# Performance work log

Hardware: AMD Instinct MI355X
Metric: run time of the kernel (lower is better)

## Reference

```python
import jax, jax.numpy as jnp
import numpy as np

N = 4096      # n_nodes
F = 512       # input_dim
R = 64        # repr_dim
H = 8         # n_heads
EPS_BIAS = 0.01
ALPHA = 0.2   # LeakyReLU negative slope
NEG_BIG = 1e16


def setup_inputs() -> dict:
    key = jax.random.key(0)
    k1, k2, k3, k4, k5 = jax.random.split(key, 5)
    node_matrix = jax.random.normal(k1, (N, F), dtype=jnp.float32)
    adjacency_matrix = (jax.random.uniform(k2, (N, N)) < 0.01).astype(jnp.float32)
    adjacency_matrix = jnp.maximum(adjacency_matrix, jnp.eye(N, dtype=jnp.float32))
    # learned parameters (xavier-ish scale)
    W = jax.random.normal(k3, (H, F, R), dtype=jnp.float32) * 0.06
    shared_attention = jax.random.normal(k4, (H, 2 * R), dtype=jnp.float32) * 0.1
    attention_biases = jax.random.normal(k5, (N, N), dtype=jnp.float32) * 0.02
    return {
        "node_matrix": node_matrix,
        "adjacency_matrix": adjacency_matrix,
        "W": W,
        "shared_attention": shared_attention,
        "attention_biases": attention_biases,
    }


def reference(node_matrix, adjacency_matrix, W, shared_attention, attention_biases):
    # hidden_repr: [H, N, R]
    hidden = jnp.einsum('nf,hfr->hnr', node_matrix, W)
    # per-head source/destination scores: [H, N]
    a_src = jnp.einsum('hnr,hr->hn', hidden, shared_attention[:, :R])
    a_dst = jnp.einsum('hnr,hr->hn', hidden, shared_attention[:, R:])
    # broadcast-sum + trainable pair bias: [H, N, N]
    pre = a_src[:, :, None] + a_dst[:, None, :] + EPS_BIAS * attention_biases[None]
    full = jnp.where(pre >= 0, pre, ALPHA * pre)  # LeakyReLU
    # adjacency masking then row softmax
    scores = full + (-NEG_BIG * (1.0 - adjacency_matrix))[None]
    att = jax.nn.softmax(scores, axis=-1)  # [H, N, N]
    # weighted aggregation: [H, N, R]
    out = jnp.einsum('hnm,hmr->hnr', att, hidden)
    # 'concat' aggregation: [N, H*R], head h occupies columns h*R:(h+1)*R
    return jnp.transpose(out, (1, 0, 2)).reshape(N, H * R)
```

## Files before the change

### kernel.cpp

```cpp
#include <hip/hip_runtime.h>
#include <hip/hip_bf16.h>

#define NN 4096
#define FF 512
#define RR 64
#define HH 8
#define HR (HH * RR)
#define CAP 128
#define ATT_STRIDE 144

typedef short bf16x8 __attribute__((ext_vector_type(8)));
typedef float f32x4 __attribute__((ext_vector_type(4)));

__device__ __forceinline__ unsigned short f2bf(float f) {
  __hip_bfloat16 h = __float2bfloat16(f);
  return *reinterpret_cast<unsigned short*>(&h);
}
__device__ __forceinline__ float bf2f(unsigned short u) {
  union { unsigned u32; float f; } cv;
  cv.u32 = ((unsigned)u) << 16;
  return cv.f;
}

__global__ __launch_bounds__(256) void k_convert(
    const float* __restrict__ X, const float* __restrict__ W,
    unsigned short* __restrict__ Xb, unsigned short* __restrict__ BbT)
{
  const int t = blockIdx.x * 256 + threadIdx.x;
  if (t < 524288) {
    const float4 v = reinterpret_cast<const float4*>(X)[t];
    ushort4 u;
    u.x = f2bf(v.x); u.y = f2bf(v.y); u.z = f2bf(v.z); u.w = f2bf(v.w);
    reinterpret_cast<ushort4*>(Xb)[t] = u;
  } else {
    const int o = t - 524288;
    const int n = o >> 9;
    const int f = o & 511;
    const int h = n >> 6, r = n & 63;
    BbT[(size_t)n * FF + f] = f2bf(W[(size_t)h * FF * RR + (size_t)f * RR + r]);
  }
}

__global__ __launch_bounds__(256) void k_gemm_hidden(
    const unsigned short* __restrict__ Xb,
    const unsigned short* __restrict__ BbT,
    unsigned short* __restrict__ hiddenT)
{
  const int row0 = blockIdx.x * 64;
  const int n0 = blockIdx.y * 64;
  __shared__ unsigned short Als[64 * 32];
  __shared__ unsigned short Bls[64 * 32];
  const int tid = threadIdx.x;
  const int l = tid & 63;
  const int wid = tid >> 6;
  const int wr = wid >> 1, wc = wid & 1;

  f32x4 acc[2][2];
#pragma unroll
  for (int a = 0; a < 2; ++a)
#pragma unroll
    for (int b = 0; b < 2; ++b) acc[a][b] = (f32x4){0.f, 0.f, 0.f, 0.f};

  const int srow = tid >> 2;
  const int skel = (tid & 3) * 8;

  for (int k0 = 0; k0 < FF; k0 += 32) {
    const int4 av = *reinterpret_cast<const int4*>(
        &Xb[(size_t)(row0 + srow) * FF + k0 + skel]);
    const int4 bv = *reinterpret_cast<const int4*>(
        &BbT[(size_t)(n0 + srow) * FF + k0 + skel]);
    __syncthreads();
    *reinterpret_cast<int4*>(&Als[tid * 8]) = av;
    *reinterpret_cast<int4*>(&Bls[tid * 8]) = bv;
    __syncthreads();

    const int ka = (l >> 4) * 8;
    const bf16x8 a0 = *reinterpret_cast<const bf16x8*>(&Als[(32 * wr + 0  + (l & 15)) * 32 + ka]);
    const bf16x8 a1 = *reinterpret_cast<const bf16x8*>(&Als[(32 * wr + 16 + (l & 15)) * 32 + ka]);
    const bf16x8 b0 = *reinterpret_cast<const bf16x8*>(&Bls[(32 * wc + 0  + (l & 15)) * 32 + ka]);
    const bf16x8 b1 = *reinterpret_cast<const bf16x8*>(&Bls[(32 * wc + 16 + (l & 15)) * 32 + ka]);
    acc[0][0] = __builtin_amdgcn_mfma_f32_16x16x32_bf16(a0, b0, acc[0][0], 0, 0, 0);
    acc[0][1] = __builtin_amdgcn_mfma_f32_16x16x32_bf16(a0, b1, acc[0][1], 0, 0, 0);
    acc[1][0] = __builtin_amdgcn_mfma_f32_16x16x32_bf16(a1, b0, acc[1][0], 0, 0, 0);
    acc[1][1] = __builtin_amdgcn_mfma_f32_16x16x32_bf16(a1, b1, acc[1][1], 0, 0, 0);
  }

#pragma unroll
  for (int mi = 0; mi < 2; ++mi)
#pragma unroll
    for (int ni = 0; ni < 2; ++ni)
#pragma unroll
      for (int j = 0; j < 4; ++j) {
        const int rowg = row0 + 32 * wr + 16 * mi + ((l >> 4) << 2) + j;
        const int colg = n0 + 32 * wc + 16 * ni + (l & 15);
        hiddenT[(size_t)rowg * HR + colg] = f2bf(acc[mi][ni][j]);
      }
}

__global__ __launch_bounds__(256) void k_src_dst(
    const unsigned short* __restrict__ hiddenT,
    const float* __restrict__ sa,
    float* __restrict__ a_src,
    float* __restrict__ a_dstT)
{
  const int idx = blockIdx.x * 256 + threadIdx.x;
  const int h = idx & 7;
  const int n = idx >> 3;
  const unsigned short* hp = hiddenT + (size_t)n * HR + h * RR;
  const float* ss = sa + (size_t)h * 2 * RR;
  const float* sd = ss + RR;
  float s = 0.f, d = 0.f;
#pragma unroll
  for (int v = 0; v < 16; ++v) {
    const ushort4 u = reinterpret_cast<const ushort4*>(hp)[v];
    const float4 sv = reinterpret_cast<const float4*>(ss)[v];
    const float4 dv = reinterpret_cast<const float4*>(sd)[v];
    const float x0 = bf2f(u.x), x1 = bf2f(u.y), x2 = bf2f(u.z), x3 = bf2f(u.w);
    s += x0 * sv.x + x1 * sv.y + x2 * sv.z + x3 * sv.w;
    d += x0 * dv.x + x1 * dv.y + x2 * dv.z + x3 * dv.w;
  }
  a_src[(size_t)h * NN + n] = s;
  a_dstT[(size_t)n * HH + h] = d;
}

__device__ __forceinline__ unsigned nib4(const float4 v) {
  unsigned m = 0;
  if (v.x != 0.f) m |= 1u;
  if (v.y != 0.f) m |= 2u;
  if (v.z != 0.f) m |= 4u;
  if (v.w != 0.f) m |= 8u;
  return m;
}

__global__ __launch_bounds__(256) void k_compact(
    const float* __restrict__ adj,
    int* __restrict__ colsG,
    int* __restrict__ cnts)
{
  const int tid = threadIdx.x;
  const int lane = tid & 63;
  const int row = blockIdx.x * 4 + (tid >> 6);
  const float* arow = adj + (size_t)row * NN;

  unsigned long long pm = 0;
  {
    float4 buf[8];
#pragma unroll
    for (int c = 0; c < 8; ++c)
      buf[c] = *reinterpret_cast<const float4*>(&arow[c * 256 + (lane << 2)]);
#pragma unroll
    for (int c = 0; c < 8; ++c)
      pm |= (unsigned long long)nib4(buf[c]) << (4 * c);
#pragma unroll
    for (int c = 0; c < 8; ++c)
      buf[c] = *reinterpret_cast<const float4*>(&arow[(c + 8) * 256 + (lane << 2)]);
#pragma unroll
    for (int c = 0; c < 8; ++c)
      pm |= (unsigned long long)nib4(buf[c]) << (4 * c + 32);
  }
  const int cnt = __popcll(pm);

  int pfx = cnt;
#pragma unroll
  for (int off = 1; off < 64; off <<= 1) {
    const int o = __shfl_up(pfx, off);
    if (lane >= off) pfx += o;
  }

  int pos = pfx - cnt;
  unsigned long long m = pm;
  int* cg = colsG + (size_t)row * CAP;
  while (m) {
    const int b = (int)__builtin_ctzll(m);
    m &= m - 1;
    if (pos < CAP) cg[pos] = ((b >> 2) << 8) + (lane << 2) + (b & 3);
    ++pos;
  }
  if (lane == 63) cnts[row] = pfx < CAP ? pfx : CAP;
}

__global__ __launch_bounds__(128) void k_gat_row(
    const int* __restrict__ colsG,
    const int* __restrict__ cnts,
    const float* __restrict__ bias,
    const float* __restrict__ a_src,
    const float* __restrict__ a_dstT,
    const unsigned short* __restrict__ hiddenT,
    float* __restrict__ out)
{
  const int i = blockIdx.x;
  const int tid = threadIdx.x;

  __shared__ __align__(16) float att[HH][ATT_STRIDE];
  __shared__ int cols[CAP];

  const int count = cnts[i];
  const float* brow = bias + (size_t)i * NN;

  float asrc[HH];
#pragma unroll
  for (int h = 0; h < HH; ++h) asrc[h] = a_src[(size_t)h * NN + i];

  if (tid < count) {
    const int c = colsG[(size_t)i * CAP + tid];
    cols[tid] = c;
    const float b = 0.01f * brow[c];
    const float4 d0 = *reinterpret_cast<const float4*>(&a_dstT[(size_t)c * HH]);
    const float4 d1 = *reinterpret_cast<const float4*>(&a_dstT[(size_t)c * HH + 4]);
    float s;
    s = asrc[0] + d0.x + b; att[0][tid] = (s >= 0.f) ? s : 0.2f * s;
    s = asrc[1] + d0.y + b; att[1][tid] = (s >= 0.f) ? s : 0.2f * s;
    s = asrc[2] + d0.z + b; att[2][tid] = (s >= 0.f) ? s : 0.2f * s;
    s = asrc[3] + d0.w + b; att[3][tid] = (s >= 0.f) ? s : 0.2f * s;
    s = asrc[4] + d1.x + b; att[4][tid] = (s >= 0.f) ? s : 0.2f * s;
    s = asrc[5] + d1.y + b; att[5][tid] = (s >= 0.f) ? s : 0.2f * s;
    s = asrc[6] + d1.z + b; att[6][tid] = (s >= 0.f) ? s : 0.2f * s;
    s = asrc[7] + d1.w + b; att[7][tid] = (s >= 0.f) ? s : 0.2f * s;
  }
  __syncthreads();

  {
    const int g = tid >> 4;
    const int l16 = tid & 15;
    float* arow_h = att[g];
    float m = -3.0e38f;
    for (int t = l16; t < count; t += 16) m = fmaxf(m, arow_h[t]);
#pragma unroll
    for (int o = 8; o >= 1; o >>= 1) m = fmaxf(m, __shfl_xor(m, o));
    float ssum = 0.f;
    for (int t = l16; t < count; t += 16) {
      const float e = expf(arow_h[t] - m);
      arow_h[t] = e;
      ssum += e;
    }
#pragma unroll
    for (int o = 8; o >= 1; o >>= 1) ssum += __shfl_xor(ssum, o);
    const float inv = 1.0f / ssum;
    for (int t = l16; t < count; t += 16) arow_h[t] *= inv;
  }
  __syncthreads();

  {
    const int o0 = tid << 2;
    const float* attrow = att[tid >> 4];
    const unsigned short* hb = hiddenT + o0;
    float4 acc = make_float4(0.f, 0.f, 0.f, 0.f);
    int t = 0;
    for (; t + 4 <= count; t += 4) {
      const int4 c4 = *reinterpret_cast<const int4*>(&cols[t]);
      const float4 a4 = *reinterpret_cast<const float4*>(&attrow[t]);
#pragma unroll
      for (int j = 0; j < 4; ++j) {
        const int c = (j == 0) ? c4.x : (j == 1) ? c4.y : (j == 2) ? c4.z : c4.w;
        const float a = (j == 0) ? a4.x : (j == 1) ? a4.y : (j == 2) ? a4.z : a4.w;
        const ushort4 u = *reinterpret_cast<const ushort4*>(hb + (size_t)c * HR);
        acc.x += a * bf2f(u.x); acc.y += a * bf2f(u.y);
        acc.z += a * bf2f(u.z); acc.w += a * bf2f(u.w);
      }
    }
    for (; t < count; ++t) {
      const int c = cols[t];
      const float a = attrow[t];
      const ushort4 u = *reinterpret_cast<const ushort4*>(hb + (size_t)c * HR);
      acc.x += a * bf2f(u.x); acc.y += a * bf2f(u.y);
      acc.z += a * bf2f(u.z); acc.w += a * bf2f(u.w);
    }
    *reinterpret_cast<float4*>(&out[(size_t)i * HR + o0]) = acc;
  }
}

extern "C" void kernel_launch(void* const* d_in, const int* in_sizes, int n_in,
                              void* d_out, int out_size, void* d_ws, size_t ws_size,
                              hipStream_t stream) {
  const float* X    = (const float*)d_in[0];
  const float* adj  = (const float*)d_in[1];
  const float* W    = (const float*)d_in[2];
  const float* sa   = (const float*)d_in[3];
  const float* bias = (const float*)d_in[4];
  float* out = (float*)d_out;

  unsigned short* hiddenT = (unsigned short*)d_ws;
  unsigned short* Xb  = hiddenT + (size_t)NN * HR;
  unsigned short* BbT = Xb + (size_t)NN * FF;
  float* a_src  = (float*)(BbT + (size_t)HR * FF);
  float* a_dstT = a_src + (size_t)HH * NN;
  int* cnts     = (int*)(a_dstT + (size_t)NN * HH);
  int* colsG    = (int*)Xb;

  k_convert<<<dim3(3072), 256, 0, stream>>>(X, W, Xb, BbT);
  k_gemm_hidden<<<dim3(NN / 64, HR / 64), 256, 0, stream>>>(Xb, BbT, hiddenT);
  k_src_dst<<<dim3(128), 256, 0, stream>>>(hiddenT, sa, a_src, a_dstT);
  k_compact<<<dim3(NN / 4), 256, 0, stream>>>(adj, colsG, cnts);
  k_gat_row<<<dim3(NN), 128, 0, stream>>>(colsG, cnts, bias, a_src, a_dstT, hiddenT, out);
}
```

Before: 55.23 us.

## Fuse adjacency compaction with conversion, fold score dots into GEMM, split aggregation

Adjacency compaction, X conversion and W transpose now run in one launch. The W transpose is tiled through shared memory so its reads and writes are coalesced. The per-head source/destination score dot products move into the GEMM epilogue, which removes one kernel and a re-read of hidden. The row aggregation kernel doubles to 256 threads, splitting the neighbour list in halves and reducing the two halves through shared memory. Together this cuts launches and adds occupancy in the gather, at the cost of extra shuffles and an added barrier.

```diff
diff --git a/kernel.cpp b/kernel.cpp
--- a/kernel.cpp
+++ b/kernel.cpp
@@ -21,35 +21,109 @@
   cv.u32 = ((unsigned)u) << 16;
   return cv.f;
 }
-
-__global__ __launch_bounds__(256) void k_convert(
+__device__ __forceinline__ unsigned nib4(const float4 v) {
+  unsigned m = 0;
+  if (v.x != 0.f) m |= 1u;
+  if (v.y != 0.f) m |= 2u;
+  if (v.z != 0.f) m |= 4u;
+  if (v.w != 0.f) m |= 8u;
+  return m;
+}
+
+__global__ __launch_bounds__(256) void k_stream(
     const float* __restrict__ X, const float* __restrict__ W,
-    unsigned short* __restrict__ Xb, unsigned short* __restrict__ BbT)
+    const float* __restrict__ adj,
+    unsigned short* __restrict__ Xb, unsigned short* __restrict__ BbT,
+    int* __restrict__ colsG, int* __restrict__ cnts)
 {
-  const int t = blockIdx.x * 256 + threadIdx.x;
-  if (t < 524288) {
+  __shared__ unsigned short wt[64][68];
+  const int b = blockIdx.x;
+  const int tid = threadIdx.x;
+
+  if (b < 1024) {
+    const int lane = tid & 63;
+    const int row = b * 4 + (tid >> 6);
+    const float* arow = adj + (size_t)row * NN;
+    unsigned long long pm = 0;
+    {
+      float4 buf[8];
+#pragma unroll
+      for (int c = 0; c < 8; ++c)
+        buf[c] = *reinterpret_cast<const float4*>(&arow[c * 256 + (lane << 2)]);
+#pragma unroll
+      for (int c = 0; c < 8; ++c)
+        pm |= (unsigned long long)nib4(buf[c]) << (4 * c);
+#pragma unroll
+      for (int c = 0; c < 8; ++c)
+        buf[c] = *reinterpret_cast<const float4*>(&arow[(c + 8) * 256 + (lane << 2)]);
+#pragma unroll
+      for (int c = 0; c < 8; ++c)
+        pm |= (unsigned long long)nib4(buf[c]) << (4 * c + 32);
+    }
+    const int cnt = __popcll(pm);
+    int pfx = cnt;
+#pragma unroll
+    for (int off = 1; off < 64; off <<= 1) {
+      const int o = __shfl_up(pfx, off);
+      if (lane >= off) pfx += o;
+    }
+    int pos = pfx - cnt;
+    unsigned long long m = pm;
+    int* cg = colsG + (size_t)row * CAP;
+    while (m) {
+      const int bit = (int)__builtin_ctzll(m);
+      m &= m - 1;
+      if (pos < CAP) cg[pos] = ((bit >> 2) << 8) + (lane << 2) + (bit & 3);
+      ++pos;
+    }
+    if (lane == 63) cnts[row] = pfx < CAP ? pfx : CAP;
+  } else if (b < 3072) {
+    const int t = (b - 1024) * 256 + tid;
     const float4 v = reinterpret_cast<const float4*>(X)[t];
     ushort4 u;
     u.x = f2bf(v.x); u.y = f2bf(v.y); u.z = f2bf(v.z); u.w = f2bf(v.w);
     reinterpret_cast<ushort4*>(Xb)[t] = u;
   } else {
-    const int o = t - 524288;
-    const int n = o >> 9;
-    const int f = o & 511;
-    const int h = n >> 6, r = n & 63;
-    BbT[(size_t)n * FF + f] = f2bf(W[(size_t)h * FF * RR + (size_t)f * RR + r]);
+    const int b2 = b - 3072;
+    const int h = b2 >> 3;
+    const int f0 = (b2 & 7) << 6;
+    const int fr = tid >> 2;
+    const int rq = (tid & 3) << 4;
+    const float* wp = W + (size_t)h * FF * RR + (size_t)(f0 + fr) * RR + rq;
+#pragma unroll
+    for (int v = 0; v < 4; ++v) {
+      const float4 x = *reinterpret_cast<const float4*>(wp + v * 4);
+      wt[rq + v * 4 + 0][fr] = f2bf(x.x);
+      wt[rq + v * 4 + 1][fr] = f2bf(x.y);
+      wt[rq + v * 4 + 2][fr] = f2bf(x.z);
+      wt[rq + v * 4 + 3][fr] = f2bf(x.w);
+    }
+    __syncthreads();
+    const int r = tid >> 2;
+    unsigned short* op = BbT + (size_t)(h * 64 + r) * FF + f0 + ((tid & 3) << 4);
+    int4 w0, w1;
+    w0 = *reinterpret_cast<const int4*>(&wt[r][(tid & 3) << 4]);
+    w1 = *reinterpret_cast<const int4*>(&wt[r][((tid & 3) << 4) + 8]);
+    *reinterpret_cast<int4*>(op) = w0;
+    *reinterpret_cast<int4*>(op + 8) = w1;
   }
 }
 
 __global__ __launch_bounds__(256) void k_gemm_hidden(
     const unsigned short* __restrict__ Xb,
     const unsigned short* __restrict__ BbT,
-    unsigned short* __restrict__ hiddenT)
+    const float* __restrict__ sa,
+    unsigned short* __restrict__ hiddenT,
+    float* __restrict__ a_src,
+    float* __restrict__ a_dstT)
 {
   const int row0 = blockIdx.x * 64;
-  const int n0 = blockIdx.y * 64;
+  const int h = blockIdx.y;
+  const int n0 = h * 64;
   __shared__ unsigned short Als[64 * 32];
   __shared__ unsigned short Bls[64 * 32];
+  __shared__ float redS[64][2];
+  __shared__ float redD[64][2];
   const int tid = threadIdx.x;
   const int l = tid & 63;
   const int wid = tid >> 6;
@@ -59,7 +133,7 @@
 #pragma unroll
   for (int a = 0; a < 2; ++a)
 #pragma unroll
-    for (int b = 0; b < 2; ++b) acc[a][b] = (f32x4){0.f, 0.f, 0.f, 0.f};
+    for (int bb = 0; bb < 2; ++bb) acc[a][bb] = (f32x4){0.f, 0.f, 0.f, 0.f};
 
   const int srow = tid >> 2;
   const int skel = (tid & 3) * 8;
@@ -85,101 +159,52 @@
     acc[1][1] = __builtin_amdgcn_mfma_f32_16x16x32_bf16(a1, b1, acc[1][1], 0, 0, 0);
   }
 
+  const int lg = l >> 4;
+  const int lc = l & 15;
+
 #pragma unroll
   for (int mi = 0; mi < 2; ++mi)
 #pragma unroll
     for (int ni = 0; ni < 2; ++ni)
 #pragma unroll
       for (int j = 0; j < 4; ++j) {
-        const int rowg = row0 + 32 * wr + 16 * mi + ((l >> 4) << 2) + j;
-        const int colg = n0 + 32 * wc + 16 * ni + (l & 15);
+        const int rowg = row0 + 32 * wr + 16 * mi + (lg << 2) + j;
+        const int colg = n0 + 32 * wc + 16 * ni + lc;
         hiddenT[(size_t)rowg * HR + colg] = f2bf(acc[mi][ni][j]);
       }
-}
-
-__global__ __launch_bounds__(256) void k_src_dst(
-    const unsigned short* __restrict__ hiddenT,
-    const float* __restrict__ sa,
-    float* __restrict__ a_src,
-    float* __restrict__ a_dstT)
-{
-  const int idx = blockIdx.x * 256 + threadIdx.x;
-  const int h = idx & 7;
-  const int n = idx >> 3;
-  const unsigned short* hp = hiddenT + (size_t)n * HR + h * RR;
-  const float* ss = sa + (size_t)h * 2 * RR;
-  const float* sd = ss + RR;
-  float s = 0.f, d = 0.f;
-#pragma unroll
-  for (int v = 0; v < 16; ++v) {
-    const ushort4 u = reinterpret_cast<const ushort4*>(hp)[v];
-    const float4 sv = reinterpret_cast<const float4*>(ss)[v];
-    const float4 dv = reinterpret_cast<const float4*>(sd)[v];
-    const float x0 = bf2f(u.x), x1 = bf2f(u.y), x2 = bf2f(u.z), x3 = bf2f(u.w);
-    s += x0 * sv.x + x1 * sv.y + x2 * sv.z + x3 * sv.w;
-    d += x0 * dv.x + x1 * dv.y + x2 * dv.z + x3 * dv.w;
-  }
-  a_src[(size_t)h * NN + n] = s;
-  a_dstT[(size_t)n * HH + h] = d;
-}
-
-__device__ __forceinline__ unsigned nib4(const float4 v) {
-  unsigned m = 0;
-  if (v.x != 0.f) m |= 1u;
-  if (v.y != 0.f) m |= 2u;
-  if (v.z != 0.f) m |= 4u;
-  if (v.w != 0.f) m |= 8u;
-  return m;
-}
-
-__global__ __launch_bounds__(256) void k_compact(
-    const float* __restrict__ adj,
-    int* __restrict__ colsG,
-    int* __restrict__ cnts)
-{
-  const int tid = threadIdx.x;
-  const int lane = tid & 63;
-  const int row = blockIdx.x * 4 + (tid >> 6);
-  const float* arow = adj + (size_t)row * NN;
-
-  unsigned long long pm = 0;
-  {
-    float4 buf[8];
-#pragma unroll
-    for (int c = 0; c < 8; ++c)
-      buf[c] = *reinterpret_cast<const float4*>(&arow[c * 256 + (lane << 2)]);
-#pragma unroll
-    for (int c = 0; c < 8; ++c)
-      pm |= (unsigned long long)nib4(buf[c]) << (4 * c);
-#pragma unroll
-    for (int c = 0; c < 8; ++c)
-      buf[c] = *reinterpret_cast<const float4*>(&arow[(c + 8) * 256 + (lane << 2)]);
-#pragma unroll
-    for (int c = 0; c < 8; ++c)
-      pm |= (unsigned long long)nib4(buf[c]) << (4 * c + 32);
-  }
-  const int cnt = __popcll(pm);
-
-  int pfx = cnt;
-#pragma unroll
-  for (int off = 1; off < 64; off <<= 1) {
-    const int o = __shfl_up(pfx, off);
-    if (lane >= off) pfx += o;
-  }
-
-  int pos = pfx - cnt;
-  unsigned long long m = pm;
-  int* cg = colsG + (size_t)row * CAP;
-  while (m) {
-    const int b = (int)__builtin_ctzll(m);
-    m &= m - 1;
-    if (pos < CAP) cg[pos] = ((b >> 2) << 8) + (lane << 2) + (b & 3);
-    ++pos;
-  }
-  if (lane == 63) cnts[row] = pfx < CAP ? pfx : CAP;
-}
-
-__global__ __launch_bounds__(128) void k_gat_row(
+
+  float sS[2], sD[2];
+#pragma unroll
+  for (int ni = 0; ni < 2; ++ni) {
+    const int col = 32 * wc + 16 * ni + lc;
+    sS[ni] = sa[(size_t)h * 2 * RR + col];
+    sD[ni] = sa[(size_t)h * 2 * RR + RR + col];
+  }
+#pragma unroll
+  for (int mi = 0; mi < 2; ++mi)
+#pragma unroll
+    for (int j = 0; j < 4; ++j) {
+      float ps = acc[mi][0][j] * sS[0] + acc[mi][1][j] * sS[1];
+      float pd = acc[mi][0][j] * sD[0] + acc[mi][1][j] * sD[1];
+#pragma unroll
+      for (int off = 8; off >= 1; off >>= 1) {
+        ps += __shfl_xor(ps, off);
+        pd += __shfl_xor(pd, off);
+      }
+      if (lc == 0) {
+        const int rl = 32 * wr + 16 * mi + (lg << 2) + j;
+        redS[rl][wc] = ps;
+        redD[rl][wc] = pd;
+      }
+    }
+  __syncthreads();
+  if (tid < 64) {
+    a_src[(size_t)h * NN + row0 + tid] = redS[tid][0] + redS[tid][1];
+    a_dstT[(size_t)(row0 + tid) * HH + h] = redD[tid][0] + redD[tid][1];
+  }
+}
+
+__global__ __launch_bounds__(256) void k_gat_row(
     const int* __restrict__ colsG,
     const int* __restrict__ cnts,
     const float* __restrict__ bias,
@@ -193,6 +218,7 @@
 
   __shared__ __align__(16) float att[HH][ATT_STRIDE];
   __shared__ int cols[CAP];
+  __shared__ __align__(16) float accred[2][HR];
 
   const int count = cnts[i];
   const float* brow = bias + (size_t)i * NN;
@@ -220,52 +246,61 @@
   __syncthreads();
 
   {
-    const int g = tid >> 4;
-    const int l16 = tid & 15;
+    const int g = tid >> 5;
+    const int l = tid & 31;
     float* arow_h = att[g];
     float m = -3.0e38f;
-    for (int t = l16; t < count; t += 16) m = fmaxf(m, arow_h[t]);
-#pragma unroll
-    for (int o = 8; o >= 1; o >>= 1) m = fmaxf(m, __shfl_xor(m, o));
+    for (int t = l; t < count; t += 32) m = fmaxf(m, arow_h[t]);
+#pragma unroll
+    for (int o = 16; o >= 1; o >>= 1) m = fmaxf(m, __shfl_xor(m, o));
     float ssum = 0.f;
-    for (int t = l16; t < count; t += 16) {
+    for (int t = l; t < count; t += 32) {
       const float e = expf(arow_h[t] - m);
       arow_h[t] = e;
       ssum += e;
     }
 #pragma unroll
-    for (int o = 8; o >= 1; o >>= 1) ssum += __shfl_xor(ssum, o);
+    for (int o = 16; o >= 1; o >>= 1) ssum += __shfl_xor(ssum, o);
     const float inv = 1.0f / ssum;
-    for (int t = l16; t < count; t += 16) arow_h[t] *= inv;
+    for (int t = l; t < count; t += 32) arow_h[t] *= inv;
   }
   __syncthreads();
 
   {
-    const int o0 = tid << 2;
-    const float* attrow = att[tid >> 4];
+    const int g2 = tid >> 7;
+    const int o0 = (tid & 127) << 2;
+    const float* attrow = att[o0 >> 6];
     const unsigned short* hb = hiddenT + o0;
+    const int half = (count + 1) >> 1;
+    const int t0 = g2 * half;
+    const int t1 = (g2 == 0) ? half : count;
     float4 acc = make_float4(0.f, 0.f, 0.f, 0.f);
-    int t = 0;
-    for (; t + 4 <= count; t += 4) {
-      const int4 c4 = *reinterpret_cast<const int4*>(&cols[t]);
-      const float4 a4 = *reinterpret_cast<const float4*>(&attrow[t]);
-#pragma unroll
-      for (int j = 0; j < 4; ++j) {
-        const int c = (j == 0) ? c4.x : (j == 1) ? c4.y : (j == 2) ? c4.z : c4.w;
-        const float a = (j == 0) ? a4.x : (j == 1) ? a4.y : (j == 2) ? a4.z : a4.w;
-        const ushort4 u = *reinterpret_cast<const ushort4*>(hb + (size_t)c * HR);
-        acc.x += a * bf2f(u.x); acc.y += a * bf2f(u.y);
-        acc.z += a * bf2f(u.z); acc.w += a * bf2f(u.w);
-      }
-    }
-    for (; t < count; ++t) {
+    int t = t0;
+    for (; t + 2 <= t1; t += 2) {
+      const int ca = cols[t], cb = cols[t + 1];
+      const float aa = attrow[t], ab = attrow[t + 1];
+      const ushort4 ua = *reinterpret_cast<const ushort4*>(hb + (size_t)ca * HR);
+      const ushort4 ub = *reinterpret_cast<const ushort4*>(hb + (size_t)cb * HR);
+      acc.x += aa * bf2f(ua.x) + ab * bf2f(ub.x);
+      acc.y += aa * bf2f(ua.y) + ab * bf2f(ub.y);
+      acc.z += aa * bf2f(ua.z) + ab * bf2f(ub.z);
+      acc.w += aa * bf2f(ua.w) + ab * bf2f(ub.w);
+    }
+    if (t < t1) {
       const int c = cols[t];
       const float a = attrow[t];
       const ushort4 u = *reinterpret_cast<const ushort4*>(hb + (size_t)c * HR);
       acc.x += a * bf2f(u.x); acc.y += a * bf2f(u.y);
       acc.z += a * bf2f(u.z); acc.w += a * bf2f(u.w);
     }
-    *reinterpret_cast<float4*>(&out[(size_t)i * HR + o0]) = acc;
+    *reinterpret_cast<float4*>(&accred[g2][o0]) = acc;
+  }
+  __syncthreads();
+  {
+    const int o = tid << 1;
+    const float2 r = make_float2(accred[0][o] + accred[1][o],
+                                 accred[0][o + 1] + accred[1][o + 1]);
+    *reinterpret_cast<float2*>(&out[(size_t)i * HR + o]) = r;
   }
 }
 
@@ -285,11 +320,9 @@
   float* a_src  = (float*)(BbT + (size_t)HR * FF);
   float* a_dstT = a_src + (size_t)HH * NN;
   int* cnts     = (int*)(a_dstT + (size_t)NN * HH);
-  int* colsG    = (int*)Xb;
-
-  k_convert<<<dim3(3072), 256, 0, stream>>>(X, W, Xb, BbT);
-  k_gemm_hidden<<<dim3(NN / 64, HR / 64), 256, 0, stream>>>(Xb, BbT, hiddenT);
-  k_src_dst<<<dim3(128), 256, 0, stream>>>(hiddenT, sa, a_src, a_dstT);
-  k_compact<<<dim3(NN / 4), 256, 0, stream>>>(adj, colsG, cnts);
-  k_gat_row<<<dim3(NN), 128, 0, stream>>>(colsG, cnts, bias, a_src, a_dstT, hiddenT, out);
-}
+  int* colsG    = cnts + NN;
+
+  k_stream<<<dim3(3136), 256, 0, stream>>>(X, W, adj, Xb, BbT, colsG, cnts);
+  k_gemm_hidden<<<dim3(NN / 64, HH), 256, 0, stream>>>(Xb, BbT, sa, hiddenT, a_src, a_dstT);
+  k_gat_row<<<dim3(NN), 256, 0, stream>>>(colsG, cnts, bias, a_src, a_dstT, hiddenT, out);
+}
```

Measured after the change: 48.20 us. 1.15x faster.
